# Performance work log

Measured on AMD Instinct MI355X. Metric: run time of the kernel, lower is better.

The kernel has to match this reference:

```python
import jax, jax.numpy as jnp
import numpy as np

N, D, E, K, CAP = 16384, 1024, 64, 2, 640

def setup_inputs() -> dict:
    key = jax.random.key(0)
    k1, k2, k3 = jax.random.split(key, 3)
    x = jax.random.normal(k1, (N, D), dtype=jnp.float32)
    Wr = jax.random.normal(k2, (D, E), dtype=jnp.float32) / np.sqrt(D)
    br = jnp.zeros((E,), dtype=jnp.float32)
    We = jax.random.normal(k3, (E, D, D), dtype=jnp.float32) / np.sqrt(D)
    return {"x": x, "Wr": Wr, "br": br, "We": We, "k": K, "capacity": CAP}

def _route(x, Wr, br, k, num_experts):
    logits = x @ Wr + br                                  # [N, E]
    top_k_vals, top_k_idxs = jax.lax.top_k(logits, k)     # [N, k]
    gates = jax.nn.softmax(top_k_vals, axis=-1)           # [N, k]
    # flatten k-major like the original: transpose((1,0)).flatten()
    flat = top_k_idxs.T.reshape(-1)                       # [k*N]
    expert_mask = (flat[:, None] == jnp.arange(num_experts)).astype(jnp.int32)
    buffer_idxs = jnp.cumsum(expert_mask, axis=0) * expert_mask - 1  # [k*N, E]
    buffer_idxs = buffer_idxs.reshape(k, -1, num_experts)            # [k, N, E]
    dispatch_idxs = buffer_idxs.transpose(2, 0, 1).max(axis=1)       # [E, N]
    combine_idxs = buffer_idxs.max(axis=-1).T                        # [N, k]
    return gates, top_k_idxs, dispatch_idxs, combine_idxs

def reference(x, Wr, br, We, k, capacity):
    num_experts = Wr.shape[1]
    gates, top_k_idxs, dispatch_idxs, combine_idxs = _route(x, Wr, br, k, num_experts)
    # dispatch: scatter tokens into per-expert capacity buffers; unassigned (-1)
    # and overflow (>= capacity) tokens land in the dropped slot `capacity`.
    d_idx = jnp.where((dispatch_idxs < 0) | (dispatch_idxs > capacity), capacity, dispatch_idxs)
    def scatter_one(idx):
        return jnp.zeros((capacity + 1, x.shape[-1]), x.dtype).at[idx].set(x)[:-1]
    dispatched = jax.vmap(scatter_one)(d_idx)             # [E, C, D]
    # per-expert linear (the wrap()/vmap-ed expert), grouped GEMM
    expert_out = jax.nn.relu(jnp.einsum('ecd,edh->ech', dispatched, We))
    # combine: gather back, pad row `capacity` yields zeros for dropped tokens
    padded = jnp.pad(expert_out, ((0, 0), (0, 1), (0, 0)))
    c_idx = jnp.where((combine_idxs < 0) | (combine_idxs > capacity), capacity, combine_idxs)
    combined = padded[top_k_idxs, c_idx]                  # [N, k, D]
    return jnp.einsum('nk,nkd->nd', gates, combined)      # [N, D]
```

## Files before the change

kernel.cpp:

```cpp
#include <hip/hip_runtime.h>
#include <hip/hip_bf16.h>
#include <cstdint>
#include <cstddef>

#define N_TOK 16384
#define DIM   1024
#define NEXP  64
#define CAPACITY 640

typedef __bf16 bf16x8 __attribute__((ext_vector_type(8)));
typedef float  f32x4  __attribute__((ext_vector_type(4)));

__device__ __forceinline__ unsigned short f2bf(float f) {
    union { float f; unsigned int u; } a; a.f = f;
    unsigned int r = a.u + 0x7FFFu + ((a.u >> 16) & 1u);
    return (unsigned short)(r >> 16);
}

__global__ __launch_bounds__(256) void router_kernel(
    const float* __restrict__ x, const float* __restrict__ Wr,
    const float* __restrict__ br, unsigned short* __restrict__ xb,
    int* __restrict__ top2i, float* __restrict__ gates2)
{
    __shared__ float xs[64][68];
    __shared__ float wT[64][68];
    const int tid = threadIdx.x;
    const int t0  = blockIdx.x * 64;
    const int tm  = tid >> 4;
    const int te  = tid & 15;

    float acc[4][4];
#pragma unroll
    for (int i = 0; i < 4; i++)
#pragma unroll
        for (int j = 0; j < 4; j++) acc[i][j] = 0.f;

    for (int ks = 0; ks < DIM; ks += 64) {
        __syncthreads();
#pragma unroll
        for (int l = 0; l < 4; l++) {
            int row = l * 16 + tm;
            int col = te * 4;
            float4 v = *(const float4*)(x + (size_t)(t0 + row) * DIM + ks + col);
            *(float4*)&xs[row][col] = v;
            ushort4 b = make_ushort4(f2bf(v.x), f2bf(v.y), f2bf(v.z), f2bf(v.w));
            *(ushort4*)(xb + (size_t)(t0 + row) * DIM + ks + col) = b;
        }
#pragma unroll
        for (int l = 0; l < 4; l++) {
            int kr = l * 16 + tm;
            int ec = te * 4;
            float4 v = *(const float4*)(Wr + (size_t)(ks + kr) * NEXP + ec);
            wT[ec + 0][kr] = v.x; wT[ec + 1][kr] = v.y;
            wT[ec + 2][kr] = v.z; wT[ec + 3][kr] = v.w;
        }
        __syncthreads();
#pragma unroll 4
        for (int kk = 0; kk < 64; kk += 4) {
            float4 xv[4], wv[4];
#pragma unroll
            for (int i = 0; i < 4; i++) xv[i] = *(float4*)&xs[tm + i * 16][kk];
#pragma unroll
            for (int j = 0; j < 4; j++) wv[j] = *(float4*)&wT[te + j * 16][kk];
#pragma unroll
            for (int i = 0; i < 4; i++)
#pragma unroll
                for (int j = 0; j < 4; j++)
                    acc[i][j] += xv[i].x * wv[j].x + xv[i].y * wv[j].y +
                                 xv[i].z * wv[j].z + xv[i].w * wv[j].w;
        }
    }
    __syncthreads();
#pragma unroll
    for (int i = 0; i < 4; i++)
#pragma unroll
        for (int j = 0; j < 4; j++)
            xs[tm + i * 16][te + j * 16] = acc[i][j] + br[te + j * 16];
    __syncthreads();
    if (tid < 64) {
        int n = t0 + tid;
        float v1 = -1e30f, v2 = -1e30f; int i1 = 0, i2 = 0;
        for (int e = 0; e < 64; e++) {
            float v = xs[tid][e];
            if (v > v1)      { v2 = v1; i2 = i1; v1 = v; i1 = e; }
            else if (v > v2) { v2 = v;  i2 = e; }
        }
        float g0 = 1.f / (1.f + expf(v2 - v1));
        top2i[n * 2 + 0] = i1; top2i[n * 2 + 1] = i2;
        gates2[n * 2 + 0] = g0; gates2[n * 2 + 1] = 1.f - g0;
    }
}

__global__ __launch_bounds__(256) void hist_kernel(
    const int* __restrict__ top2i, int* __restrict__ hist)
{
    __shared__ int cnt[NEXP];
    int tid = threadIdx.x;
    if (tid < NEXP) cnt[tid] = 0;
    __syncthreads();
    int p = blockIdx.x * 256 + tid;
    int k = p >> 14, n = p & 16383;
    int e = top2i[n * 2 + k];
    atomicAdd(&cnt[e], 1);
    __syncthreads();
    if (tid < NEXP) hist[blockIdx.x * NEXP + tid] = cnt[tid];
}

__global__ __launch_bounds__(64) void scan_kernel(
    const int* __restrict__ hist, int* __restrict__ pre, int* __restrict__ cntc)
{
    int e = threadIdx.x;
    int run = 0;
#pragma unroll 8
    for (int c = 0; c < 128; c++) {
        pre[c * NEXP + e] = run;
        run += hist[c * NEXP + e];
    }
    cntc[e] = run < CAPACITY ? run : CAPACITY;
}

__global__ __launch_bounds__(64) void rank_kernel(
    const int* __restrict__ top2i, const float* __restrict__ gates2,
    const int* __restrict__ pre, int* __restrict__ list_tok,
    float* __restrict__ list_gate)
{
    int lane = threadIdx.x;
    int c = blockIdx.x;
    int cnt_reg = pre[c * NEXP + lane];
    unsigned long long below = (1ull << lane) - 1ull;
    for (int r = 0; r < 4; r++) {
        int p = c * 256 + r * 64 + lane;
        int k = p >> 14, n = p & 16383;
        int e = top2i[n * 2 + k];
        int slot = 0;
#pragma unroll 1
        for (int q = 0; q < NEXP; q++) {
            unsigned long long mask = __ballot(e == q);
            int base = __shfl(cnt_reg, q);
            if (e == q) slot = base + __popcll(mask & below);
            if (lane == q) cnt_reg += (int)__popcll(mask);
        }
        if (slot < CAPACITY) {
            list_tok[e * CAPACITY + slot]  = n;
            list_gate[e * CAPACITY + slot] = gates2[n * 2 + k];
        }
    }
}

__global__ __launch_bounds__(256) void convert_we(
    const float* __restrict__ We, unsigned short* __restrict__ WeB)
{
    const int b   = blockIdx.x;
    const int e   = b >> 7;
    const int nt  = (b >> 4) & 7;
    const int ksi = b & 15;
    __shared__ __align__(16) unsigned short T[64][132];
    const int tid = threadIdx.x;
    const int tc  = (tid & 31) * 4;
    const int tr  = tid >> 5;
    const float* src = We + ((size_t)e << 20) + (size_t)(ksi * 64) * DIM + nt * 128;
#pragma unroll
    for (int l = 0; l < 8; l++) {
        int dr = l * 8 + tr;
        float4 v = *(const float4*)(src + (size_t)dr * DIM + tc);
        ushort4 u = make_ushort4(f2bf(v.x), f2bf(v.y), f2bf(v.z), f2bf(v.w));
        *(ushort4*)&T[dr][tc] = u;
    }
    __syncthreads();
    unsigned short* dst = WeB + ((size_t)b << 13);
#pragma unroll
    for (int i = 0; i < 4; i++) {
        int p = i * 256 + tid;
        int kq = p >> 7, col = p & 127;
        unsigned int w0 = (unsigned int)T[kq * 8 + 0][col] | ((unsigned int)T[kq * 8 + 1][col] << 16);
        unsigned int w1 = (unsigned int)T[kq * 8 + 2][col] | ((unsigned int)T[kq * 8 + 3][col] << 16);
        unsigned int w2 = (unsigned int)T[kq * 8 + 4][col] | ((unsigned int)T[kq * 8 + 5][col] << 16);
        unsigned int w3 = (unsigned int)T[kq * 8 + 6][col] | ((unsigned int)T[kq * 8 + 7][col] << 16);
        *(uint4*)(dst + (size_t)p * 8) = make_uint4(w0, w1, w2, w3);
    }
}

__global__ __launch_bounds__(256) void moe_gemm2(
    const unsigned short* __restrict__ xb, const unsigned short* __restrict__ WeB,
    const int* __restrict__ list_tok, const float* __restrict__ list_gate,
    const int* __restrict__ cntc, float* __restrict__ out)
{
    const int bid = blockIdx.x;
    const int e   = bid / 40;
    const int rem = bid % 40;
    const int mt  = rem >> 3;
    const int nt  = rem & 7;
    const int cnt = cntc[e];
    if (mt * 128 >= cnt) return;
    int valid = cnt - mt * 128; if (valid > 128) valid = 128;

    __shared__ __align__(16) unsigned short As[8 * 128 * 8];
    __shared__ __align__(16) unsigned short Bs[8 * 128 * 8];
    __shared__ int   tok_s[128];
    __shared__ float gate_s[128];

    const int tid = threadIdx.x;
    if (tid < 128) {
        int slot = mt * 128 + tid;
        bool v = tid < valid;
        tok_s[tid]  = v ? list_tok[e * CAPACITY + slot]  : list_tok[e * CAPACITY];
        gate_s[tid] = v ? list_gate[e * CAPACITY + slot] : 0.f;
    }
    __syncthreads();

    const int arow  = tid & 127;
    const int ahalf = tid >> 7;
    const unsigned short* aG = xb + (size_t)tok_s[arow] * DIM + ahalf * 8;
    const unsigned short* bG = WeB + ((size_t)(e * 8 + nt) * 16) * 8192 + (size_t)tid * 8;

    const int wv   = tid >> 6;
    const int lane = tid & 63;
    const int wm = wv >> 1, wn = wv & 1;
    const int fm = lane & 15, kq = lane >> 4;

    f32x4 acc[4][4];
#pragma unroll
    for (int i = 0; i < 4; i++)
#pragma unroll
        for (int j = 0; j < 4; j++) acc[i][j] = (f32x4){0.f, 0.f, 0.f, 0.f};

    for (int ksi = 0; ksi < 16; ksi++) {
        __syncthreads();
#pragma unroll
        for (int i = 0; i < 4; i++) {
            const int ldsOff = (i * 256 + wv * 64) * 8;
            __builtin_amdgcn_global_load_lds(
                (const __attribute__((address_space(1))) unsigned int*)(aG + ksi * 64 + i * 16),
                (__attribute__((address_space(3))) unsigned int*)(As + ldsOff), 16, 0, 0);
            __builtin_amdgcn_global_load_lds(
                (const __attribute__((address_space(1))) unsigned int*)(bG + (size_t)ksi * 8192 + i * 2048),
                (__attribute__((address_space(3))) unsigned int*)(Bs + ldsOff), 16, 0, 0);
        }
        __syncthreads();
#pragma unroll
        for (int kk = 0; kk < 2; kk++) {
            union { uint4 u; bf16x8 v; } fa[4], fb[4];
#pragma unroll
            for (int i = 0; i < 4; i++)
                fa[i].u = *(const uint4*)(As + ((kk * 4 + kq) * 128 + wm * 64 + i * 16 + fm) * 8);
#pragma unroll
            for (int j = 0; j < 4; j++)
                fb[j].u = *(const uint4*)(Bs + ((kk * 4 + kq) * 128 + wn * 64 + j * 16 + fm) * 8);
#pragma unroll
            for (int i = 0; i < 4; i++)
#pragma unroll
                for (int j = 0; j < 4; j++)
                    acc[i][j] = __builtin_amdgcn_mfma_f32_16x16x32_bf16(
                        fa[i].v, fb[j].v, acc[i][j], 0, 0, 0);
        }
    }

    const int col0 = nt * 128 + wn * 64 + fm;
#pragma unroll
    for (int i = 0; i < 4; i++) {
        int rbase = wm * 64 + i * 16 + kq * 4;
#pragma unroll
        for (int j = 0; j < 4; j++) {
            int col = col0 + j * 16;
#pragma unroll
            for (int r = 0; r < 4; r++) {
                int row = rbase + r;
                if (row < valid) {
                    float v = acc[i][j][r];
                    v = fmaxf(v, 0.f) * gate_s[row];
                    atomicAdd(out + (size_t)tok_s[row] * DIM + col, v);
                }
            }
        }
    }
}

#define MT 128
#define NT 128
#define BK 32
#define LDA 36

__global__ __launch_bounds__(256) void moe_gemm(
    const unsigned short* __restrict__ xb, const float* __restrict__ We,
    const int* __restrict__ list_tok, const float* __restrict__ list_gate,
    const int* __restrict__ cntc, float* __restrict__ out)
{
    const int bid = blockIdx.x;
    const int e   = bid / 40;
    const int rem = bid % 40;
    const int mt  = rem >> 3;
    const int nt  = rem & 7;
    const int cnt = cntc[e];
    if (mt * MT >= cnt) return;
    int valid = cnt - mt * MT; if (valid > MT) valid = MT;

    __shared__ unsigned short As[MT * LDA];
    __shared__ unsigned short Bs[NT * LDA];
    __shared__ int   tok_s[MT];
    __shared__ float gate_s[MT];

    const int tid = threadIdx.x;
    if (tid < MT) {
        int slot = mt * MT + tid;
        bool v = tid < valid;
        tok_s[tid]  = v ? list_tok[e * CAPACITY + slot]  : list_tok[e * CAPACITY];
        gate_s[tid] = v ? list_gate[e * CAPACITY + slot] : 0.f;
    }
    __syncthreads();

    const int arow = tid >> 1, ah = tid & 1;
    const unsigned short* aptr = xb + (size_t)tok_s[arow] * DIM + ah * 16;
    const int bn0 = (tid & 31) * 4;
    const int bkr = (tid >> 5) * 4;
    const float* bptr = We + (size_t)e * DIM * DIM + (size_t)bkr * DIM + nt * NT + bn0;

    f32x4 acc[4][4];
#pragma unroll
    for (int i = 0; i < 4; i++)
#pragma unroll
        for (int j = 0; j < 4; j++) acc[i][j] = (f32x4){0.f, 0.f, 0.f, 0.f};

    const int lane = tid & 63, wave = tid >> 6;
    const int wm = wave >> 1, wn = wave & 1;
    const int fm = lane & 15, kq = lane >> 4;

    for (int ks = 0; ks < DIM; ks += BK) {
        __syncthreads();
        uint4 a0 = *(const uint4*)(aptr + ks);
        uint4 a1 = *(const uint4*)(aptr + ks + 8);
        {
            unsigned short* d = &As[arow * LDA + ah * 16];
            *(uint2*)(d + 0)  = make_uint2(a0.x, a0.y);
            *(uint2*)(d + 4)  = make_uint2(a0.z, a0.w);
            *(uint2*)(d + 8)  = make_uint2(a1.x, a1.y);
            *(uint2*)(d + 12) = make_uint2(a1.z, a1.w);
        }
        {
            float4 b[4];
#pragma unroll
            for (int j = 0; j < 4; j++)
                b[j] = *(const float4*)(bptr + (size_t)(ks + j) * DIM);
            union { float4 v; float f[4]; } u0, u1, u2, u3;
            u0.v = b[0]; u1.v = b[1]; u2.v = b[2]; u3.v = b[3];
#pragma unroll
            for (int cc = 0; cc < 4; cc++) {
                unsigned int lo = (unsigned int)f2bf(u0.f[cc]) | ((unsigned int)f2bf(u1.f[cc]) << 16);
                unsigned int hi = (unsigned int)f2bf(u2.f[cc]) | ((unsigned int)f2bf(u3.f[cc]) << 16);
                *(uint2*)&Bs[(bn0 + cc) * LDA + bkr] = make_uint2(lo, hi);
            }
        }
        __syncthreads();
        union { uint2 u[2]; bf16x8 v; } fa[4], fb[4];
#pragma unroll
        for (int i = 0; i < 4; i++) {
            const unsigned short* s = &As[(wm * 64 + i * 16 + fm) * LDA + kq * 8];
            fa[i].u[0] = *(const uint2*)(s);
            fa[i].u[1] = *(const uint2*)(s + 4);
        }
#pragma unroll
        for (int j = 0; j < 4; j++) {
            const unsigned short* s = &Bs[(wn * 64 + j * 16 + fm) * LDA + kq * 8];
            fb[j].u[0] = *(const uint2*)(s);
            fb[j].u[1] = *(const uint2*)(s + 4);
        }
#pragma unroll
        for (int i = 0; i < 4; i++)
#pragma unroll
            for (int j = 0; j < 4; j++)
                acc[i][j] = __builtin_amdgcn_mfma_f32_16x16x32_bf16(
                    fa[i].v, fb[j].v, acc[i][j], 0, 0, 0);
    }

    const int col0 = nt * NT + wn * 64 + fm;
#pragma unroll
    for (int i = 0; i < 4; i++) {
        int rbase = wm * 64 + i * 16 + kq * 4;
#pragma unroll
        for (int j = 0; j < 4; j++) {
            int col = col0 + j * 16;
#pragma unroll
            for (int r = 0; r < 4; r++) {
                int row = rbase + r;
                if (row < valid) {
                    float v = acc[i][j][r];
                    v = fmaxf(v, 0.f) * gate_s[row];
                    atomicAdd(out + (size_t)tok_s[row] * DIM + col, v);
                }
            }
        }
    }
}

extern "C" void kernel_launch(void* const* d_in, const int* in_sizes, int n_in,
                              void* d_out, int out_size, void* d_ws, size_t ws_size,
                              hipStream_t stream)
{
    const float* x  = (const float*)d_in[0];
    const float* Wr = (const float*)d_in[1];
    const float* br = (const float*)d_in[2];
    const float* We = (const float*)d_in[3];
    float* out = (float*)d_out;

    char* ws = (char*)d_ws;
    size_t off = 0;
    unsigned short* xb = (unsigned short*)(ws + off); off += (size_t)N_TOK * DIM * 2;
    int*   top2i     = (int*)(ws + off);   off += (size_t)N_TOK * 2 * 4;
    float* gates2    = (float*)(ws + off); off += (size_t)N_TOK * 2 * 4;
    int*   hist      = (int*)(ws + off);   off += 128 * NEXP * 4;
    int*   pre       = (int*)(ws + off);   off += 128 * NEXP * 4;
    int*   cntc      = (int*)(ws + off);   off += NEXP * 4;
    int*   list_tok  = (int*)(ws + off);   off += NEXP * CAPACITY * 4;
    float* list_gate = (float*)(ws + off); off += NEXP * CAPACITY * 4;
    off = (off + 255) & ~(size_t)255;
    unsigned short* WeB = (unsigned short*)(ws + off);
    size_t need = off + (size_t)NEXP * DIM * DIM * 2;

    const bool fast = ws_size >= need;

    hipMemsetAsync(out, 0, (size_t)N_TOK * DIM * 4, stream);
    if (fast)
        convert_we<<<NEXP * 8 * 16, 256, 0, stream>>>(We, WeB);
    router_kernel<<<N_TOK / 64, 256, 0, stream>>>(x, Wr, br, xb, top2i, gates2);
    hist_kernel<<<128, 256, 0, stream>>>(top2i, hist);
    scan_kernel<<<1, 64, 0, stream>>>(hist, pre, cntc);
    rank_kernel<<<128, 64, 0, stream>>>(top2i, gates2, pre, list_tok, list_gate);
    if (fast)
        moe_gemm2<<<NEXP * 40, 256, 0, stream>>>(xb, WeB, list_tok, list_gate, cntc, out);
    else
        moe_gemm<<<NEXP * 40, 256, 0, stream>>>(xb, We, list_tok, list_gate, cntc, out);
}
```

Measured before the change: 743.6 us.

## Fuse router, weight conversion, output zeroing and histogram; double-buffer expert GEMM

Merges the router, the fp32-to-bf16 expert weight conversion and the output zeroing into one launch by splitting the grid into block ranges. The histogram is built with atomics inside the router, and the separate scan is folded into the rank kernel, which recomputes each chunk's prefix itself. The expert GEMM now double-buffers its LDS tiles so the next K-slice loads while the current one computes. The aim is fewer launches and serial gaps and hidden load latency in the GEMM, at the cost of global atomics on the histogram, a redundant prefix loop in rank, and twice the LDS in the GEMM.

```diff
diff --git a/kernel.cpp b/kernel.cpp
--- a/kernel.cpp
+++ b/kernel.cpp
@@ -17,14 +17,58 @@
     return (unsigned short)(r >> 16);
 }
 
-__global__ __launch_bounds__(256) void router_kernel(
+__global__ __launch_bounds__(256) void router_convert(
     const float* __restrict__ x, const float* __restrict__ Wr,
-    const float* __restrict__ br, unsigned short* __restrict__ xb,
-    int* __restrict__ top2i, float* __restrict__ gates2)
+    const float* __restrict__ br, const float* __restrict__ We,
+    unsigned short* __restrict__ xb, unsigned short* __restrict__ WeB,
+    int* __restrict__ top2i, float* __restrict__ gates2,
+    int* __restrict__ hist, float* __restrict__ out)
 {
-    __shared__ float xs[64][68];
-    __shared__ float wT[64][68];
+    __shared__ __align__(16) float smem[2][64][68];
     const int tid = threadIdx.x;
+
+    if (blockIdx.x >= 8448) {
+        const int z = blockIdx.x - 8448;
+        float4* o = (float4*)(out + (size_t)z * 32768);
+        const float4 zero = make_float4(0.f, 0.f, 0.f, 0.f);
+#pragma unroll
+        for (int l = 0; l < 32; l++) o[l * 256 + tid] = zero;
+        return;
+    }
+
+    if (blockIdx.x >= 256) {
+        const int b   = blockIdx.x - 256;
+        const int e   = b >> 7;
+        const int nt  = (b >> 4) & 7;
+        const int ksi = b & 15;
+        unsigned short (*T)[132] = (unsigned short (*)[132])smem;
+        const int tc  = (tid & 31) * 4;
+        const int tr  = tid >> 5;
+        const float* src = We + ((size_t)e << 20) + (size_t)(ksi * 64) * DIM + nt * 128;
+#pragma unroll
+        for (int l = 0; l < 8; l++) {
+            int dr = l * 8 + tr;
+            float4 v = *(const float4*)(src + (size_t)dr * DIM + tc);
+            ushort4 u = make_ushort4(f2bf(v.x), f2bf(v.y), f2bf(v.z), f2bf(v.w));
+            *(ushort4*)&T[dr][tc] = u;
+        }
+        __syncthreads();
+        unsigned short* dst = WeB + ((size_t)b << 13);
+#pragma unroll
+        for (int i = 0; i < 4; i++) {
+            int p = i * 256 + tid;
+            int kq = p >> 7, col = p & 127;
+            unsigned int w0 = (unsigned int)T[kq * 8 + 0][col] | ((unsigned int)T[kq * 8 + 1][col] << 16);
+            unsigned int w1 = (unsigned int)T[kq * 8 + 2][col] | ((unsigned int)T[kq * 8 + 3][col] << 16);
+            unsigned int w2 = (unsigned int)T[kq * 8 + 4][col] | ((unsigned int)T[kq * 8 + 5][col] << 16);
+            unsigned int w3 = (unsigned int)T[kq * 8 + 6][col] | ((unsigned int)T[kq * 8 + 7][col] << 16);
+            *(uint4*)(dst + (size_t)p * 8) = make_uint4(w0, w1, w2, w3);
+        }
+        return;
+    }
+
+    float (*xs)[68] = smem[0];
+    float (*wT)[68] = smem[1];
     const int t0  = blockIdx.x * 64;
     const int tm  = tid >> 4;
     const int te  = tid & 15;
@@ -88,45 +132,21 @@
         float g0 = 1.f / (1.f + expf(v2 - v1));
         top2i[n * 2 + 0] = i1; top2i[n * 2 + 1] = i2;
         gates2[n * 2 + 0] = g0; gates2[n * 2 + 1] = 1.f - g0;
-    }
-}
-
-__global__ __launch_bounds__(256) void hist_kernel(
-    const int* __restrict__ top2i, int* __restrict__ hist)
-{
-    __shared__ int cnt[NEXP];
-    int tid = threadIdx.x;
-    if (tid < NEXP) cnt[tid] = 0;
-    __syncthreads();
-    int p = blockIdx.x * 256 + tid;
-    int k = p >> 14, n = p & 16383;
-    int e = top2i[n * 2 + k];
-    atomicAdd(&cnt[e], 1);
-    __syncthreads();
-    if (tid < NEXP) hist[blockIdx.x * NEXP + tid] = cnt[tid];
-}
-
-__global__ __launch_bounds__(64) void scan_kernel(
-    const int* __restrict__ hist, int* __restrict__ pre, int* __restrict__ cntc)
-{
-    int e = threadIdx.x;
-    int run = 0;
-#pragma unroll 8
-    for (int c = 0; c < 128; c++) {
-        pre[c * NEXP + e] = run;
-        run += hist[c * NEXP + e];
-    }
-    cntc[e] = run < CAPACITY ? run : CAPACITY;
+        atomicAdd(&hist[(n >> 8) * NEXP + i1], 1);
+        atomicAdd(&hist[(64 + (n >> 8)) * NEXP + i2], 1);
+    }
 }
 
 __global__ __launch_bounds__(64) void rank_kernel(
     const int* __restrict__ top2i, const float* __restrict__ gates2,
-    const int* __restrict__ pre, int* __restrict__ list_tok,
-    float* __restrict__ list_gate)
+    const int* __restrict__ hist, int* __restrict__ list_tok,
+    float* __restrict__ list_gate, int* __restrict__ cntc)
 {
     int lane = threadIdx.x;
     int c = blockIdx.x;
-    int cnt_reg = pre[c * NEXP + lane];
+    int cnt_reg = 0;
+#pragma unroll 4
+    for (int cc = 0; cc < c; cc++) cnt_reg += hist[cc * NEXP + lane];
     unsigned long long below = (1ull << lane) - 1ull;
     for (int r = 0; r < 4; r++) {
         int p = c * 256 + r * 64 + lane;
@@ -145,42 +165,10 @@
             list_gate[e * CAPACITY + slot] = gates2[n * 2 + k];
         }
     }
-}
-
-__global__ __launch_bounds__(256) void convert_we(
-    const float* __restrict__ We, unsigned short* __restrict__ WeB)
-{
-    const int b   = blockIdx.x;
-    const int e   = b >> 7;
-    const int nt  = (b >> 4) & 7;
-    const int ksi = b & 15;
-    __shared__ __align__(16) unsigned short T[64][132];
-    const int tid = threadIdx.x;
-    const int tc  = (tid & 31) * 4;
-    const int tr  = tid >> 5;
-    const float* src = We + ((size_t)e << 20) + (size_t)(ksi * 64) * DIM + nt * 128;
-#pragma unroll
-    for (int l = 0; l < 8; l++) {
-        int dr = l * 8 + tr;
-        float4 v = *(const float4*)(src + (size_t)dr * DIM + tc);
-        ushort4 u = make_ushort4(f2bf(v.x), f2bf(v.y), f2bf(v.z), f2bf(v.w));
-        *(ushort4*)&T[dr][tc] = u;
-    }
-    __syncthreads();
-    unsigned short* dst = WeB + ((size_t)b << 13);
-#pragma unroll
-    for (int i = 0; i < 4; i++) {
-        int p = i * 256 + tid;
-        int kq = p >> 7, col = p & 127;
-        unsigned int w0 = (unsigned int)T[kq * 8 + 0][col] | ((unsigned int)T[kq * 8 + 1][col] << 16);
-        unsigned int w1 = (unsigned int)T[kq * 8 + 2][col] | ((unsigned int)T[kq * 8 + 3][col] << 16);
-        unsigned int w2 = (unsigned int)T[kq * 8 + 4][col] | ((unsigned int)T[kq * 8 + 5][col] << 16);
-        unsigned int w3 = (unsigned int)T[kq * 8 + 6][col] | ((unsigned int)T[kq * 8 + 7][col] << 16);
-        *(uint4*)(dst + (size_t)p * 8) = make_uint4(w0, w1, w2, w3);
-    }
-}
-
-__global__ __launch_bounds__(256) void moe_gemm2(
+    if (c == 127) cntc[lane] = cnt_reg < CAPACITY ? cnt_reg : CAPACITY;
+}
+
+__global__ __launch_bounds__(256) void moe_gemm3(
     const unsigned short* __restrict__ xb, const unsigned short* __restrict__ WeB,
     const int* __restrict__ list_tok, const float* __restrict__ list_gate,
     const int* __restrict__ cntc, float* __restrict__ out)
@@ -194,8 +182,8 @@
     if (mt * 128 >= cnt) return;
     int valid = cnt - mt * 128; if (valid > 128) valid = 128;
 
-    __shared__ __align__(16) unsigned short As[8 * 128 * 8];
-    __shared__ __align__(16) unsigned short Bs[8 * 128 * 8];
+    __shared__ __align__(16) unsigned short As[2][8192];
+    __shared__ __align__(16) unsigned short Bs[2][8192];
     __shared__ int   tok_s[128];
     __shared__ float gate_s[128];
 
@@ -224,28 +212,28 @@
 #pragma unroll
         for (int j = 0; j < 4; j++) acc[i][j] = (f32x4){0.f, 0.f, 0.f, 0.f};
 
-    for (int ksi = 0; ksi < 16; ksi++) {
-        __syncthreads();
+    auto stage = [&](int buf, int ksi) {
 #pragma unroll
         for (int i = 0; i < 4; i++) {
             const int ldsOff = (i * 256 + wv * 64) * 8;
             __builtin_amdgcn_global_load_lds(
                 (const __attribute__((address_space(1))) unsigned int*)(aG + ksi * 64 + i * 16),
-                (__attribute__((address_space(3))) unsigned int*)(As + ldsOff), 16, 0, 0);
+                (__attribute__((address_space(3))) unsigned int*)(&As[buf][ldsOff]), 16, 0, 0);
             __builtin_amdgcn_global_load_lds(
                 (const __attribute__((address_space(1))) unsigned int*)(bG + (size_t)ksi * 8192 + i * 2048),
-                (__attribute__((address_space(3))) unsigned int*)(Bs + ldsOff), 16, 0, 0);
-        }
-        __syncthreads();
+                (__attribute__((address_space(3))) unsigned int*)(&Bs[buf][ldsOff]), 16, 0, 0);
+        }
+    };
+    auto compute = [&](int buf) {
 #pragma unroll
         for (int kk = 0; kk < 2; kk++) {
             union { uint4 u; bf16x8 v; } fa[4], fb[4];
 #pragma unroll
             for (int i = 0; i < 4; i++)
-                fa[i].u = *(const uint4*)(As + ((kk * 4 + kq) * 128 + wm * 64 + i * 16 + fm) * 8);
+                fa[i].u = *(const uint4*)(&As[buf][((kk * 4 + kq) * 128 + wm * 64 + i * 16 + fm) * 8]);
 #pragma unroll
             for (int j = 0; j < 4; j++)
-                fb[j].u = *(const uint4*)(Bs + ((kk * 4 + kq) * 128 + wn * 64 + j * 16 + fm) * 8);
+                fb[j].u = *(const uint4*)(&Bs[buf][((kk * 4 + kq) * 128 + wn * 64 + j * 16 + fm) * 8]);
 #pragma unroll
             for (int i = 0; i < 4; i++)
 #pragma unroll
@@ -253,7 +241,19 @@
                     acc[i][j] = __builtin_amdgcn_mfma_f32_16x16x32_bf16(
                         fa[i].v, fb[j].v, acc[i][j], 0, 0, 0);
         }
-    }
+    };
+
+    stage(0, 0);
+    __syncthreads();
+    int cur = 0;
+#pragma unroll 1
+    for (int ksi = 1; ksi < 16; ksi++) {
+        stage(cur ^ 1, ksi);
+        compute(cur);
+        __syncthreads();
+        cur ^= 1;
+    }
+    compute(cur);
 
     const int col0 = nt * 128 + wn * 64 + fm;
 #pragma unroll
@@ -407,7 +407,6 @@
     int*   top2i     = (int*)(ws + off);   off += (size_t)N_TOK * 2 * 4;
     float* gates2    = (float*)(ws + off); off += (size_t)N_TOK * 2 * 4;
     int*   hist      = (int*)(ws + off);   off += 128 * NEXP * 4;
-    int*   pre       = (int*)(ws + off);   off += 128 * NEXP * 4;
     int*   cntc      = (int*)(ws + off);   off += NEXP * 4;
     int*   list_tok  = (int*)(ws + off);   off += NEXP * CAPACITY * 4;
     float* list_gate = (float*)(ws + off); off += NEXP * CAPACITY * 4;
@@ -417,15 +416,21 @@
 
     const bool fast = ws_size >= need;
 
-    hipMemsetAsync(out, 0, (size_t)N_TOK * DIM * 4, stream);
-    if (fast)
-        convert_we<<<NEXP * 8 * 16, 256, 0, stream>>>(We, WeB);
-    router_kernel<<<N_TOK / 64, 256, 0, stream>>>(x, Wr, br, xb, top2i, gates2);
-    hist_kernel<<<128, 256, 0, stream>>>(top2i, hist);
-    scan_kernel<<<1, 64, 0, stream>>>(hist, pre, cntc);
-    rank_kernel<<<128, 64, 0, stream>>>(top2i, gates2, pre, list_tok, list_gate);
-    if (fast)
-        moe_gemm2<<<NEXP * 40, 256, 0, stream>>>(xb, WeB, list_tok, list_gate, cntc, out);
-    else
-        moe_gemm<<<NEXP * 40, 256, 0, stream>>>(xb, We, list_tok, list_gate, cntc, out);
-}
+    hipMemsetAsync(hist, 0, 128 * NEXP * 4, stream);
+    if (fast) {
+        router_convert<<<8960, 256, 0, stream>>>(x, Wr, br, We, xb, WeB,
+                                                 top2i, gates2, hist, out);
+        rank_kernel<<<128, 64, 0, stream>>>(top2i, gates2, hist,
+                                            list_tok, list_gate, cntc);
+        moe_gemm3<<<NEXP * 40, 256, 0, stream>>>(xb, WeB, list_tok, list_gate,
+                                                 cntc, out);
+    } else {
+        hipMemsetAsync(out, 0, (size_t)N_TOK * DIM * 4, stream);
+        router_convert<<<256, 256, 0, stream>>>(x, Wr, br, We, xb, xb,
+                                                top2i, gates2, hist, out);
+        rank_kernel<<<128, 64, 0, stream>>>(top2i, gates2, hist,
+                                            list_tok, list_gate, cntc);
+        moe_gemm<<<NEXP * 40, 256, 0, stream>>>(xb, We, list_tok, list_gate,
+                                                cntc, out);
+    }
+}
```

Result: faster. 680.3 us (-8.5%).
